# Optimization experiments

Measured on AMD Instinct MI355X. Metric: run time of the kernel, lower is better.

The kernel has to match this reference:

```python
import jax, jax.numpy as jnp
import numpy as np

RADIUS = 1
N_POINTS = 8


def lbp(x, radius=RADIUS, n_points=N_POINTS):
    """skimage-style 'default' LBP applied per pixel of an NCHW batch.

    For each of P points on a circle of radius R, bilinearly sample the
    neighbor (zero outside the image, matching skimage's constant mode),
    compare >= center, and bit-pack with weights 2**p.
    Offsets follow skimage: row = -R*sin(theta), col = R*cos(theta).
    """
    B, C, H, W = x.shape
    angles = 2.0 * np.pi * np.arange(n_points) / n_points
    drs = np.round(-radius * np.sin(angles), 8)
    dcs = np.round(radius * np.cos(angles), 8)
    pad = int(np.ceil(radius)) + 1
    xp = jnp.pad(x, ((0, 0), (0, 0), (pad, pad), (pad, pad)))  # zeros outside

    code = jnp.zeros_like(x)
    for p in range(n_points):
        dr, dc = float(drs[p]), float(dcs[p])
        r0, c0 = int(np.floor(dr)), int(np.floor(dc))
        fr, fc = dr - r0, dc - c0  # fractional parts in [0,1)

        def win(ri, ci):
            rs, cs = pad + r0 + ri, pad + c0 + ci
            return jax.lax.slice(xp, (0, 0, rs, cs), (B, C, rs + H, cs + W))

        # bilinear sample of the shifted neighborhood (constant-0 boundary)
        v = ((1 - fr) * (1 - fc) * win(0, 0)
             + (1 - fr) * fc * win(0, 1)
             + fr * (1 - fc) * win(1, 0)
             + fr * fc * win(1, 1))
        code = code + float(2 ** p) * (v >= x).astype(x.dtype)
    return code


def setup_inputs() -> dict:
    key = jax.random.key(0)
    x = jax.random.uniform(key, (16, 64, 224, 224), dtype=jnp.float32)
    return {"x": x}


def reference(x):
    return lbp(x)
```

## Files before the change

### kernel.cpp

```cpp
#include <hip/hip_runtime.h>
#include <math.h>

#define HH 224
#define WW 224
#define PLANES (16 * 64)
#define QPLANES (PLANES / 2)
#define TILE_H 8
#define TILES_X (WW / 4)
#define TILES_Y (HH / TILE_H)
#define TILES_PER_PLANE (TILES_X * TILES_Y)
#define TOTAL_THREADS (QPLANES * TILES_PER_PLANE)

struct LbpWeights {
    float w1[4];
    float w3[4];
    float w5[4];
    float w7[4];
};

__global__ __launch_bounds__(256, 3) void lbp_kernel(const float* __restrict__ x,
                                                     float* __restrict__ out,
                                                     LbpWeights wt) {
    int tid = blockIdx.x * 256 + threadIdx.x;

    int q = tid / TILES_PER_PLANE;
    int t = tid - q * TILES_PER_PLANE;
    int tr = t / TILES_X;
    int tc = t - tr * TILES_X;
    int r0 = tr * TILE_H, c0 = tc * 4;

    const float* pb0 = x + (size_t)(2 * q) * (HH * WW);

    bool cm = (c0 > 0), cp = (c0 + 4 < WW);
    int cl_off = cm ? -1 : 0;
    int cr_off = cp ? 4 : 3;

    float a0[TILE_H + 2][6];
    float a1[TILE_H + 2][6];
#pragma unroll
    for (int i = 0; i < TILE_H + 2; i++) {
        int rr = r0 - 1 + i;
        int rrc = rr < 0 ? 0 : (rr > HH - 1 ? HH - 1 : rr);
        bool rok = (rr >= 0) && (rr < HH);
        const float* rp0 = pb0 + rrc * WW + c0;
        const float* rp1 = rp0 + HH * WW;
        float4 v0 = *(const float4*)rp0;
        float l0 = rp0[cl_off];
        float r0v = rp0[cr_off];
        float4 v1 = *(const float4*)rp1;
        float l1 = rp1[cl_off];
        float r1v = rp1[cr_off];
        a0[i][1] = rok ? v0.x : 0.0f;
        a0[i][2] = rok ? v0.y : 0.0f;
        a0[i][3] = rok ? v0.z : 0.0f;
        a0[i][4] = rok ? v0.w : 0.0f;
        a0[i][0] = (rok && cm) ? l0 : 0.0f;
        a0[i][5] = (rok && cp) ? r0v : 0.0f;
        a1[i][1] = rok ? v1.x : 0.0f;
        a1[i][2] = rok ? v1.y : 0.0f;
        a1[i][3] = rok ? v1.z : 0.0f;
        a1[i][4] = rok ? v1.w : 0.0f;
        a1[i][0] = (rok && cm) ? l1 : 0.0f;
        a1[i][5] = (rok && cp) ? r1v : 0.0f;
    }

    float* ob0 = out + (size_t)(2 * q) * (HH * WW) + r0 * WW + c0;

    auto compute = [&](const float (&a)[TILE_H + 2][6], float* ob) {
#pragma unroll
        for (int j = 0; j < TILE_H; j++) {
            float res[4];
#pragma unroll
            for (int k = 0; k < 4; k++) {
                float ctr = a[j + 1][k + 1];
                float n00 = a[j][k],     n01 = a[j][k + 1],     n02 = a[j][k + 2];
                float n10 = a[j + 1][k],                        n12 = a[j + 1][k + 2];
                float n20 = a[j + 2][k], n21 = a[j + 2][k + 1], n22 = a[j + 2][k + 2];

                float v1, v3, v5, v7;
                {
#pragma clang fp contract(off)
                    v1 = ((wt.w1[0] * n01 + wt.w1[1] * n02) + wt.w1[2] * ctr) + wt.w1[3] * n12;
                    v3 = ((wt.w3[0] * n00 + wt.w3[1] * n01) + wt.w3[2] * n10) + wt.w3[3] * ctr;
                    v5 = ((wt.w5[0] * n10 + wt.w5[1] * ctr) + wt.w5[2] * n20) + wt.w5[3] * n21;
                    v7 = ((wt.w7[0] * ctr + wt.w7[1] * n12) + wt.w7[2] * n21) + wt.w7[3] * n22;
                }

                unsigned m = 0u;
#define LBP_BIT(val)                                                   \
    asm("v_cmp_ge_f32 vcc, %1, %2\n\t"                                 \
        "v_addc_co_u32 %0, vcc, %0, %0, vcc"                           \
        : "+v"(m) : "v"(val), "v"(ctr) : "vcc")
                LBP_BIT(v7);
                LBP_BIT(n21);
                LBP_BIT(v5);
                LBP_BIT(n10);
                LBP_BIT(v3);
                LBP_BIT(n01);
                LBP_BIT(v1);
                LBP_BIT(n12);
#undef LBP_BIT
                res[k] = (float)m;
            }
            *(float4*)(ob + j * WW) = make_float4(res[0], res[1], res[2], res[3]);
        }
    };

    compute(a0, ob0);
    compute(a1, ob0 + HH * WW);
}

extern "C" void kernel_launch(void* const* d_in, const int* in_sizes, int n_in,
                              void* d_out, int out_size, void* d_ws, size_t ws_size,
                              hipStream_t stream) {
    (void)in_sizes; (void)n_in; (void)d_ws; (void)ws_size; (void)out_size;
    const float* x = (const float*)d_in[0];
    float* out = (float*)d_out;

    LbpWeights wt;
    float* slots[4] = {wt.w1, wt.w3, wt.w5, wt.w7};
    const int diag_p[4] = {1, 3, 5, 7};
    for (int i = 0; i < 4; i++) {
        int p = diag_p[i];
        double ang = (2.0 * M_PI * (double)p) / 8.0;
        double dr = rint(-sin(ang) * 1e8) / 1e8;
        double dc = rint( cos(ang) * 1e8) / 1e8;
        double r0 = floor(dr), c0 = floor(dc);
        double fr = dr - r0, fc = dc - c0;
        slots[i][0] = (float)((1.0 - fr) * (1.0 - fc));
        slots[i][1] = (float)((1.0 - fr) * fc);
        slots[i][2] = (float)(fr * (1.0 - fc));
        slots[i][3] = (float)(fr * fc);
    }

    const int block = 256;
    const int grid = TOTAL_THREADS / block;
    lbp_kernel<<<grid, block, 0, stream>>>(x, out, wt);
}
```

Measured before the change: 355.9 us.

## Stream rows through a rolling register window with software-prefetched loads per plane

Result: no change. 350.9 us (-1.4%).

```diff
diff --git a/kernel.cpp b/kernel.cpp
--- a/kernel.cpp
+++ b/kernel.cpp
@@ -4,12 +4,11 @@
 #define HH 224
 #define WW 224
 #define PLANES (16 * 64)
-#define QPLANES (PLANES / 2)
-#define TILE_H 8
+#define STRIP_H 16
 #define TILES_X (WW / 4)
-#define TILES_Y (HH / TILE_H)
-#define TILES_PER_PLANE (TILES_X * TILES_Y)
-#define TOTAL_THREADS (QPLANES * TILES_PER_PLANE)
+#define STRIPS_Y (HH / STRIP_H)
+#define STRIPS_PER_PLANE (TILES_X * STRIPS_Y)
+#define TOTAL_THREADS (PLANES * STRIPS_PER_PLANE)
 
 struct LbpWeights {
     float w1[4];
@@ -18,96 +17,107 @@
     float w7[4];
 };
 
-__global__ __launch_bounds__(256, 3) void lbp_kernel(const float* __restrict__ x,
+struct RawRow { float4 q; float l, r; };
+struct Row    { float v[6]; };
+
+__global__ __launch_bounds__(256, 6) void lbp_kernel(const float* __restrict__ x,
                                                      float* __restrict__ out,
                                                      LbpWeights wt) {
     int tid = blockIdx.x * 256 + threadIdx.x;
 
-    int q = tid / TILES_PER_PLANE;
-    int t = tid - q * TILES_PER_PLANE;
+    int plane = tid / STRIPS_PER_PLANE;
+    int t = tid - plane * STRIPS_PER_PLANE;
     int tr = t / TILES_X;
     int tc = t - tr * TILES_X;
-    int r0 = tr * TILE_H, c0 = tc * 4;
+    int r0 = tr * STRIP_H, c0 = tc * 4;
 
-    const float* pb0 = x + (size_t)(2 * q) * (HH * WW);
+    const float* pb = x + (size_t)plane * (HH * WW);
 
     bool cm = (c0 > 0), cp = (c0 + 4 < WW);
     int cl_off = cm ? -1 : 0;
     int cr_off = cp ? 4 : 3;
 
-    float a0[TILE_H + 2][6];
-    float a1[TILE_H + 2][6];
+    auto issue = [&](RawRow& s, int rr) {
+        int rrc = rr < 0 ? 0 : (rr > HH - 1 ? HH - 1 : rr);
+        const float* rp = pb + rrc * WW + c0;
+        s.q = *(const float4*)rp;
+        s.l = rp[cl_off];
+        s.r = rp[cr_off];
+    };
+    auto finalize = [&](Row& f, const RawRow& s, int rr) {
+        bool ok = (unsigned)rr < (unsigned)HH;
+        f.v[1] = ok ? s.q.x : 0.0f;
+        f.v[2] = ok ? s.q.y : 0.0f;
+        f.v[3] = ok ? s.q.z : 0.0f;
+        f.v[4] = ok ? s.q.w : 0.0f;
+        f.v[0] = (ok && cm) ? s.l : 0.0f;
+        f.v[5] = (ok && cp) ? s.r : 0.0f;
+    };
+    auto compute_row = [&](const Row& A, const Row& B, const Row& C, float* orow) {
+        float res[4];
 #pragma unroll
-    for (int i = 0; i < TILE_H + 2; i++) {
-        int rr = r0 - 1 + i;
-        int rrc = rr < 0 ? 0 : (rr > HH - 1 ? HH - 1 : rr);
-        bool rok = (rr >= 0) && (rr < HH);
-        const float* rp0 = pb0 + rrc * WW + c0;
-        const float* rp1 = rp0 + HH * WW;
-        float4 v0 = *(const float4*)rp0;
-        float l0 = rp0[cl_off];
-        float r0v = rp0[cr_off];
-        float4 v1 = *(const float4*)rp1;
-        float l1 = rp1[cl_off];
-        float r1v = rp1[cr_off];
-        a0[i][1] = rok ? v0.x : 0.0f;
-        a0[i][2] = rok ? v0.y : 0.0f;
-        a0[i][3] = rok ? v0.z : 0.0f;
-        a0[i][4] = rok ? v0.w : 0.0f;
-        a0[i][0] = (rok && cm) ? l0 : 0.0f;
-        a0[i][5] = (rok && cp) ? r0v : 0.0f;
-        a1[i][1] = rok ? v1.x : 0.0f;
-        a1[i][2] = rok ? v1.y : 0.0f;
-        a1[i][3] = rok ? v1.z : 0.0f;
-        a1[i][4] = rok ? v1.w : 0.0f;
-        a1[i][0] = (rok && cm) ? l1 : 0.0f;
-        a1[i][5] = (rok && cp) ? r1v : 0.0f;
-    }
+        for (int k = 0; k < 4; k++) {
+            float ctr = B.v[k + 1];
+            float n00 = A.v[k], n01 = A.v[k + 1], n02 = A.v[k + 2];
+            float n10 = B.v[k],                   n12 = B.v[k + 2];
+            float n20 = C.v[k], n21 = C.v[k + 1], n22 = C.v[k + 2];
 
-    float* ob0 = out + (size_t)(2 * q) * (HH * WW) + r0 * WW + c0;
+            float v1, v3, v5, v7;
+            {
+#pragma clang fp contract(off)
+                v1 = ((wt.w1[0] * n01 + wt.w1[1] * n02) + wt.w1[2] * ctr) + wt.w1[3] * n12;
+                v3 = ((wt.w3[0] * n00 + wt.w3[1] * n01) + wt.w3[2] * n10) + wt.w3[3] * ctr;
+                v5 = ((wt.w5[0] * n10 + wt.w5[1] * ctr) + wt.w5[2] * n20) + wt.w5[3] * n21;
+                v7 = ((wt.w7[0] * ctr + wt.w7[1] * n12) + wt.w7[2] * n21) + wt.w7[3] * n22;
+            }
 
-    auto compute = [&](const float (&a)[TILE_H + 2][6], float* ob) {
-#pragma unroll
-        for (int j = 0; j < TILE_H; j++) {
-            float res[4];
-#pragma unroll
-            for (int k = 0; k < 4; k++) {
-                float ctr = a[j + 1][k + 1];
-                float n00 = a[j][k],     n01 = a[j][k + 1],     n02 = a[j][k + 2];
-                float n10 = a[j + 1][k],                        n12 = a[j + 1][k + 2];
-                float n20 = a[j + 2][k], n21 = a[j + 2][k + 1], n22 = a[j + 2][k + 2];
-
-                float v1, v3, v5, v7;
-                {
-#pragma clang fp contract(off)
-                    v1 = ((wt.w1[0] * n01 + wt.w1[1] * n02) + wt.w1[2] * ctr) + wt.w1[3] * n12;
-                    v3 = ((wt.w3[0] * n00 + wt.w3[1] * n01) + wt.w3[2] * n10) + wt.w3[3] * ctr;
-                    v5 = ((wt.w5[0] * n10 + wt.w5[1] * ctr) + wt.w5[2] * n20) + wt.w5[3] * n21;
-                    v7 = ((wt.w7[0] * ctr + wt.w7[1] * n12) + wt.w7[2] * n21) + wt.w7[3] * n22;
-                }
-
-                unsigned m = 0u;
+            unsigned m = 0u;
 #define LBP_BIT(val)                                                   \
     asm("v_cmp_ge_f32 vcc, %1, %2\n\t"                                 \
         "v_addc_co_u32 %0, vcc, %0, %0, vcc"                           \
         : "+v"(m) : "v"(val), "v"(ctr) : "vcc")
-                LBP_BIT(v7);
-                LBP_BIT(n21);
-                LBP_BIT(v5);
-                LBP_BIT(n10);
-                LBP_BIT(v3);
-                LBP_BIT(n01);
-                LBP_BIT(v1);
-                LBP_BIT(n12);
+            LBP_BIT(v7);
+            LBP_BIT(n21);
+            LBP_BIT(v5);
+            LBP_BIT(n10);
+            LBP_BIT(v3);
+            LBP_BIT(n01);
+            LBP_BIT(v1);
+            LBP_BIT(n12);
 #undef LBP_BIT
-                res[k] = (float)m;
-            }
-            *(float4*)(ob + j * WW) = make_float4(res[0], res[1], res[2], res[3]);
+            res[k] = (float)m;
         }
+        *(float4*)orow = make_float4(res[0], res[1], res[2], res[3]);
     };
 
-    compute(a0, ob0);
-    compute(a1, ob0 + HH * WW);
+    Row F0, F1, F2, F3;
+    RawRow Ra, Rb;
+
+    {
+        RawRow p0; issue(p0, r0 - 1); finalize(F0, p0, r0 - 1);
+        RawRow p1; issue(p1, r0);     finalize(F1, p1, r0);
+        RawRow p2; issue(p2, r0 + 1); finalize(F2, p2, r0 + 1);
+    }
+    issue(Ra, r0 + 2);
+
+    float* ob = out + (size_t)plane * (HH * WW) + r0 * WW + c0;
+
+#pragma unroll 1
+    for (int rb = 0; rb < STRIP_H / 4; rb++) {
+        int g = rb * 4;
+        issue(Rb, r0 + g + 3);
+        finalize(F3, Ra, r0 + g + 2);
+        compute_row(F0, F1, F2, ob + (g + 0) * WW);
+        issue(Ra, r0 + g + 4);
+        finalize(F0, Rb, r0 + g + 3);
+        compute_row(F1, F2, F3, ob + (g + 1) * WW);
+        issue(Rb, r0 + g + 5);
+        finalize(F1, Ra, r0 + g + 4);
+        compute_row(F2, F3, F0, ob + (g + 2) * WW);
+        issue(Ra, r0 + g + 6);
+        finalize(F2, Rb, r0 + g + 5);
+        compute_row(F3, F0, F1, ob + (g + 3) * WW);
+    }
 }
 
 extern "C" void kernel_launch(void* const* d_in, const int* in_sizes, int n_in,
```
